# Kernel tuning notes

Measured on AMD Instinct MI355X. Metric: run time of the kernel, lower is better.

Reference implementation:

```python
import jax, jax.numpy as jnp
import numpy as np

EPS = 1e-12  # torch F.normalize eps


def _l2norm(x):
    n = jnp.sqrt(jnp.sum(x * x, axis=-1, keepdims=True))
    return x / jnp.maximum(n, EPS)


def setup_inputs() -> dict:
    key = jax.random.key(0)
    k1, k2, k3, k4 = jax.random.split(key, 4)
    Bq, Lq, Bd, Ld, H, D = 128, 32, 128, 128, 256, 128
    return {
        "query_h": jax.random.normal(k1, (Bq, Lq, H), dtype=jnp.float32),
        "doc_h": jax.random.normal(k2, (Bd, Ld, H), dtype=jnp.float32),
        "W": jax.random.normal(k3, (H, D), dtype=jnp.float32) * 0.02,
        "b": jax.random.normal(k4, (D,), dtype=jnp.float32) * 0.02,
    }


def reference(query_h, doc_h, W, b):
    # token_mapper + L2 normalize (as in embed())
    q = _l2norm(query_h @ W + b)          # [Bq, Lq, D]
    d = _l2norm(doc_h @ W + b)            # [Bd, Ld, D]
    # max_sim: cross-product bmm(doc, query^T) -> [Bq, Bd, Ld, Lq]
    scores = jnp.einsum('qsd,btd->qbts', q, d)
    # max over doc tokens (dim=1 of bmm output), sum over query tokens (dim=2)
    logits = jnp.sum(jnp.max(scores, axis=2), axis=2)  # [Bq, Bd]
    return logits
```

## Files before the change

### kernel.cpp

```cpp
#include <hip/hip_runtime.h>

typedef unsigned short u16;
typedef unsigned int u32;
typedef __attribute__((ext_vector_type(8))) short short8;
typedef __attribute__((ext_vector_type(16))) float f32x16;
typedef __attribute__((ext_vector_type(4))) float f32x4;
typedef __attribute__((ext_vector_type(4))) unsigned int u32x4;

#define H 256
#define D 128


union V16 { u32x4 u; short8 s; f32x4 f; };

static __device__ inline u32 bf16pk_rne(float a, float b) {
    u32 ua = __float_as_uint(a), ub = __float_as_uint(b);
    ua = ua + 0x7FFFu + ((ua >> 16) & 1u);
    ub = ub + 0x7FFFu + ((ub >> 16) & 1u);
    return (ua >> 16) | (ub & 0xFFFF0000u);
}

__global__ __launch_bounds__(256) void prep_w(
    const float* __restrict__ W, u16* __restrict__ whi, u16* __restrict__ wlo)
{
    const int g   = blockIdx.x * 256 + threadIdx.x;
    const int slot = g & 63;
    const int kc  = (g >> 6) & 15;
    const int nt  = g >> 10;
    const int l31 = slot >> 1;
    const int lg2 = slot & 1;
    const int k0  = kc * 16 + lg2 * 8;
    const int n   = nt * 32 + l31;

    u32 hw[4], lw[4];
    #pragma unroll
    for (int p = 0; p < 4; ++p) {
        float a = W[(size_t)(k0 + 2*p)     * D + n];
        float b = W[(size_t)(k0 + 2*p + 1) * D + n];
        u32 ua = __float_as_uint(a), ub = __float_as_uint(b);
        u32 ha = ua & 0xFFFF0000u,   hb = ub & 0xFFFF0000u;
        hw[p] = (ua >> 16) | hb;
        float la = a - __uint_as_float(ha);
        float lb = b - __uint_as_float(hb);
        u32 ra = __float_as_uint(la); ra += 0x7FFFu + ((ra >> 16) & 1u);
        u32 rb = __float_as_uint(lb); rb += 0x7FFFu + ((rb >> 16) & 1u);
        lw[p] = (ra >> 16) | (rb & 0xFFFF0000u);
    }
    u32x4 hv = {hw[0], hw[1], hw[2], hw[3]};
    u32x4 lv = {lw[0], lw[1], lw[2], lw[3]};
    *(u32x4*)&whi[(size_t)g * 8] = hv;
    *(u32x4*)&wlo[(size_t)g * 8] = lv;
}

__global__ __launch_bounds__(256) void proj_mfma(
    const float* __restrict__ Xq, const float* __restrict__ Xd,
    const float* __restrict__ bias,
    const u16* __restrict__ whi, const u16* __restrict__ wlo,
    u16* __restrict__ outq, u16* __restrict__ outd)
{
    const int tid  = threadIdx.x;
    const int wid  = tid >> 6;
    const int lane = tid & 63;
    const int l31  = lane & 31;
    const int hi   = lane >> 5;
    const int slot = l31 * 2 + hi;

    const float* X; u16* out; int trow0;
    if (blockIdx.x < 32) { X = Xq; out = outq; trow0 = blockIdx.x * 128 + wid * 32; }
    else { X = Xd; out = outd; trow0 = (blockIdx.x - 32) * 128 + wid * 32; }

    const float* xrow = X + (size_t)(trow0 + l31) * H + hi * 8;

    f32x16 acc[4];
    #pragma unroll
    for (int nt = 0; nt < 4; ++nt) acc[nt] = (f32x16){0.f};

    #pragma unroll
    for (int kc = 0; kc < 16; ++kc) {
        V16 a4, b4;
        a4.f = *(const f32x4*)(xrow + kc * 16);
        b4.f = *(const f32x4*)(xrow + kc * 16 + 4);
        float e[8];
        #pragma unroll
        for (int i = 0; i < 4; ++i) { e[i] = a4.f[i]; e[i + 4] = b4.f[i]; }

        V16 xh, xl;
        u32 xhu[4], xlu[4];
        #pragma unroll
        for (int p = 0; p < 4; ++p) {
            u32 u0 = __float_as_uint(e[2*p]), u1 = __float_as_uint(e[2*p+1]);
            u32 h0 = u0 & 0xFFFF0000u,        h1 = u1 & 0xFFFF0000u;
            xhu[p] = (u0 >> 16) | h1;
            float l0 = e[2*p]   - __uint_as_float(h0);
            float l1 = e[2*p+1] - __uint_as_float(h1);
            xlu[p] = (__float_as_uint(l0) >> 16) |
                     (__float_as_uint(l1) & 0xFFFF0000u);
        }
        xh.u = (u32x4){xhu[0], xhu[1], xhu[2], xhu[3]};
        xl.u = (u32x4){xlu[0], xlu[1], xlu[2], xlu[3]};

        #pragma unroll
        for (int nt = 0; nt < 4; ++nt) {
            V16 wh, wl;
            const size_t fo = (size_t)((nt * 16 + kc) * 64 + slot) * 8;
            wh.u = *(const u32x4*)&whi[fo];
            wl.u = *(const u32x4*)&wlo[fo];
            acc[nt] = __builtin_amdgcn_mfma_f32_32x32x16_bf16(wh.s, xh.s, acc[nt], 0, 0, 0);
            acc[nt] = __builtin_amdgcn_mfma_f32_32x32x16_bf16(wl.s, xh.s, acc[nt], 0, 0, 0);
            acc[nt] = __builtin_amdgcn_mfma_f32_32x32x16_bf16(wh.s, xl.s, acc[nt], 0, 0, 0);
        }
    }

    float ss = 0.f;
    #pragma unroll
    for (int nt = 0; nt < 4; ++nt) {
        #pragma unroll
        for (int q = 0; q < 4; ++q) {
            f32x4 b4 = *(const f32x4*)&bias[nt * 32 + q * 8 + hi * 4];
            #pragma unroll
            for (int i = 0; i < 4; ++i) {
                float v = acc[nt][q*4+i] + b4[i];
                acc[nt][q*4+i] = v;
                ss += v * v;
            }
        }
    }
    ss += __shfl_xor(ss, 32);
    const float inv = 1.0f / fmaxf(sqrtf(ss), 1e-12f);

    const size_t base = (size_t)(trow0 >> 5) * 4096;
    #pragma unroll
    for (int nt = 0; nt < 4; ++nt) {
        #pragma unroll
        for (int q = 0; q < 4; ++q) {
            float v0 = acc[nt][q*4+0] * inv, v1 = acc[nt][q*4+1] * inv;
            float v2 = acc[nt][q*4+2] * inv, v3 = acc[nt][q*4+3] * inv;
            u32 p0 = bf16pk_rne(v0, v1), p1 = bf16pk_rne(v2, v3);
            u32 r0 = __shfl_xor(p0, 32), r1 = __shfl_xor(p1, 32);
            if ((q & 1) == hi) {
                const int kc = nt * 2 + (q >> 1);
                u32x4 ck;
                if (hi == 0) ck = (u32x4){p0, p1, r0, r1};
                else         ck = (u32x4){r0, r1, p0, p1};
                *(u32x4*)&out[base + (size_t)kc * 512 + (size_t)slot * 8] = ck;
            }
        }
    }
}

__global__ __launch_bounds__(256) void maxsim_kernel(
    const u16* __restrict__ qbf, const u16* __restrict__ dbf,
    float* __restrict__ logits)
{
    __shared__ float smax[4][8][2][32];
    const int tid  = threadIdx.x;
    const int wid  = tid >> 6;
    const int lane = tid & 63;
    const int l31  = lane & 31;
    const int soff = ((lane & 31) * 2 + (lane >> 5)) * 8;

    const int qb0 = (blockIdx.x >> 4) * 2;
    const int db0 = (blockIdx.x & 15) * 8;

    short8 bq[2][8];
    #pragma unroll
    for (int qs = 0; qs < 2; ++qs) {
        const u16* qb_base = qbf + (size_t)(qb0 + qs) * 4096 + soff;
        #pragma unroll
        for (int kc = 0; kc < 8; ++kc)
            bq[qs][kc] = *(const short8*)(qb_base + kc * 512);
    }

    #pragma unroll 2
    for (int dbi = 0; dbi < 8; ++dbi) {
        const u16* dt = dbf + (size_t)((db0 + dbi) * 4 + wid) * 4096 + soff;
        short8 af[8];
        #pragma unroll
        for (int kc = 0; kc < 8; ++kc)
            af[kc] = *(const short8*)(dt + kc * 512);

        f32x16 acc0 = {0.f}, acc1 = {0.f};
        #pragma unroll
        for (int kc = 0; kc < 8; ++kc) {
            acc0 = __builtin_amdgcn_mfma_f32_32x32x16_bf16(af[kc], bq[0][kc], acc0, 0, 0, 0);
            acc1 = __builtin_amdgcn_mfma_f32_32x32x16_bf16(af[kc], bq[1][kc], acc1, 0, 0, 0);
        }

        #pragma unroll
        for (int qs = 0; qs < 2; ++qs) {
            const f32x16 a = qs ? acc1 : acc0;
            float m0 = fmaxf(a[0], a[1]),   m1 = fmaxf(a[2], a[3]);
            float m2 = fmaxf(a[4], a[5]),   m3 = fmaxf(a[6], a[7]);
            float m4 = fmaxf(a[8], a[9]),   m5 = fmaxf(a[10], a[11]);
            float m6 = fmaxf(a[12], a[13]), m7 = fmaxf(a[14], a[15]);
            float m = fmaxf(fmaxf(fmaxf(m0, m1), fmaxf(m2, m3)),
                            fmaxf(fmaxf(m4, m5), fmaxf(m6, m7)));
            m = fmaxf(m, __shfl_xor(m, 32));
            if (lane < 32) smax[wid][dbi][qs][l31] = m;
        }
    }
    __syncthreads();

    {
        const int dbi = tid >> 5;
        const int col = tid & 31;
        float v0 = fmaxf(fmaxf(smax[0][dbi][0][col], smax[1][dbi][0][col]),
                         fmaxf(smax[2][dbi][0][col], smax[3][dbi][0][col]));
        float v1 = fmaxf(fmaxf(smax[0][dbi][1][col], smax[1][dbi][1][col]),
                         fmaxf(smax[2][dbi][1][col], smax[3][dbi][1][col]));
        v0 += __shfl_xor(v0, 1);  v1 += __shfl_xor(v1, 1);
        v0 += __shfl_xor(v0, 2);  v1 += __shfl_xor(v1, 2);
        v0 += __shfl_xor(v0, 4);  v1 += __shfl_xor(v1, 4);
        v0 += __shfl_xor(v0, 8);  v1 += __shfl_xor(v1, 8);
        v0 += __shfl_xor(v0, 16); v1 += __shfl_xor(v1, 16);
        if (col == 0) {
            logits[(size_t)qb0 * 128 + db0 + dbi]       = v0;
            logits[(size_t)(qb0 + 1) * 128 + db0 + dbi] = v1;
        }
    }
}

extern "C" void kernel_launch(void* const* d_in, const int* in_sizes, int n_in,
                              void* d_out, int out_size, void* d_ws, size_t ws_size,
                              hipStream_t stream)
{
    const float* query_h = (const float*)d_in[0];
    const float* doc_h   = (const float*)d_in[1];
    const float* W       = (const float*)d_in[2];
    const float* bias    = (const float*)d_in[3];
    float* logits = (float*)d_out;

    u16* qbf = (u16*)d_ws;
    u16* dbf = qbf + (size_t)128 * 4096;
    u16* whi = dbf + (size_t)512 * 4096;
    u16* wlo = whi + (size_t)4096 * 8;

    prep_w   <<<dim3(16),   dim3(256), 0, stream>>>(W, whi, wlo);
    proj_mfma<<<dim3(160),  dim3(256), 0, stream>>>(query_h, doc_h, bias, whi, wlo, qbf, dbf);
    maxsim_kernel<<<dim3(1024), dim3(256), 0, stream>>>(qbf, dbf, logits);
}
```

Before: 105.5 us.

## Stage projection inputs through swizzled LDS and double-buffer doc fragment loads

The projection kernel now has each wavefront copy its 32 input rows into a 32 KB-per-wave shared buffer with coalesced row loads and an XOR swizzle. MFMA operands are then read from LDS instead of issuing strided per-lane global reads. The maxsim kernel is restructured to double-buffer the doc fragment registers, prefetching the next doc tile while the current one is multiplied. This trades 128 KB of LDS per block (limiting occupancy) and more registers for better global coalescing and load/compute overlap.

Measured after the change: 104.3 us. Within noise of the previous version (-1.2%).

```diff
diff --git a/kernel.cpp b/kernel.cpp
--- a/kernel.cpp
+++ b/kernel.cpp
@@ -58,6 +58,7 @@
     const u16* __restrict__ whi, const u16* __restrict__ wlo,
     u16* __restrict__ outq, u16* __restrict__ outd)
 {
+    __shared__ float xst[4][32][256];
     const int tid  = threadIdx.x;
     const int wid  = tid >> 6;
     const int lane = tid & 63;
@@ -69,20 +70,31 @@
     if (blockIdx.x < 32) { X = Xq; out = outq; trow0 = blockIdx.x * 128 + wid * 32; }
     else { X = Xd; out = outd; trow0 = (blockIdx.x - 32) * 128 + wid * 32; }
 
-    const float* xrow = X + (size_t)(trow0 + l31) * H + hi * 8;
+    {
+        float* xw = &xst[wid][0][0];
+        const float* xs0 = X + (size_t)trow0 * H;
+        #pragma unroll
+        for (int t = 0; t < 32; ++t) {
+            f32x4 v = *(const f32x4*)&xs0[(size_t)t * H + lane * 4];
+            int sl = lane ^ (t & 7);
+            *(f32x4*)&xw[t * 256 + sl * 4] = v;
+        }
+    }
 
     f32x16 acc[4];
     #pragma unroll
     for (int nt = 0; nt < 4; ++nt) acc[nt] = (f32x16){0.f};
 
+    const float* xw = &xst[wid][0][0];
     #pragma unroll
     for (int kc = 0; kc < 16; ++kc) {
-        V16 a4, b4;
-        a4.f = *(const f32x4*)(xrow + kc * 16);
-        b4.f = *(const f32x4*)(xrow + kc * 16 + 4);
+        const int g = kc * 4 + hi * 2;
+        const int sw = l31 & 7;
+        f32x4 va = *(const f32x4*)&xw[l31 * 256 + ((g ^ sw) << 2)];
+        f32x4 vb = *(const f32x4*)&xw[l31 * 256 + (((g + 1) ^ sw) << 2)];
         float e[8];
         #pragma unroll
-        for (int i = 0; i < 4; ++i) { e[i] = a4.f[i]; e[i + 4] = b4.f[i]; }
+        for (int i = 0; i < 4; ++i) { e[i] = va[i]; e[i + 4] = vb[i]; }
 
         V16 xh, xl;
         u32 xhu[4], xlu[4];
@@ -148,6 +160,39 @@
     }
 }
 
+
+#define LOAD_AF(AF, DBI)                                                       \
+    {                                                                          \
+        const u16* dt_ = dbf + (size_t)((db0 + (DBI)) * 4 + wid) * 4096 + soff;\
+        _Pragma("unroll")                                                      \
+        for (int kc = 0; kc < 8; ++kc)                                         \
+            AF[kc] = *(const short8*)(dt_ + kc * 512);                         \
+    }
+
+#define COMPUTE_AF(AF, DBI)                                                    \
+    {                                                                          \
+        f32x16 acc0 = {0.f}, acc1 = {0.f};                                     \
+        _Pragma("unroll")                                                      \
+        for (int kc = 0; kc < 8; ++kc) {                                       \
+            acc0 = __builtin_amdgcn_mfma_f32_32x32x16_bf16(AF[kc], bq[0][kc],  \
+                                                           acc0, 0, 0, 0);     \
+            acc1 = __builtin_amdgcn_mfma_f32_32x32x16_bf16(AF[kc], bq[1][kc],  \
+                                                           acc1, 0, 0, 0);     \
+        }                                                                      \
+        _Pragma("unroll")                                                      \
+        for (int qs = 0; qs < 2; ++qs) {                                       \
+            const f32x16 a = qs ? acc1 : acc0;                                 \
+            float m0 = fmaxf(a[0], a[1]),   m1 = fmaxf(a[2], a[3]);            \
+            float m2 = fmaxf(a[4], a[5]),   m3 = fmaxf(a[6], a[7]);            \
+            float m4 = fmaxf(a[8], a[9]),   m5 = fmaxf(a[10], a[11]);          \
+            float m6 = fmaxf(a[12], a[13]), m7 = fmaxf(a[14], a[15]);          \
+            float m = fmaxf(fmaxf(fmaxf(m0, m1), fmaxf(m2, m3)),               \
+                            fmaxf(fmaxf(m4, m5), fmaxf(m6, m7)));              \
+            m = fmaxf(m, __shfl_xor(m, 32));                                   \
+            if (lane < 32) smax[wid][DBI][qs][l31] = m;                        \
+        }                                                                      \
+    }
+
 __global__ __launch_bounds__(256) void maxsim_kernel(
     const u16* __restrict__ qbf, const u16* __restrict__ dbf,
     float* __restrict__ logits)
@@ -171,33 +216,14 @@
             bq[qs][kc] = *(const short8*)(qb_base + kc * 512);
     }
 
-    #pragma unroll 2
-    for (int dbi = 0; dbi < 8; ++dbi) {
-        const u16* dt = dbf + (size_t)((db0 + dbi) * 4 + wid) * 4096 + soff;
-        short8 af[8];
-        #pragma unroll
-        for (int kc = 0; kc < 8; ++kc)
-            af[kc] = *(const short8*)(dt + kc * 512);
-
-        f32x16 acc0 = {0.f}, acc1 = {0.f};
-        #pragma unroll
-        for (int kc = 0; kc < 8; ++kc) {
-            acc0 = __builtin_amdgcn_mfma_f32_32x32x16_bf16(af[kc], bq[0][kc], acc0, 0, 0, 0);
-            acc1 = __builtin_amdgcn_mfma_f32_32x32x16_bf16(af[kc], bq[1][kc], acc1, 0, 0, 0);
-        }
-
-        #pragma unroll
-        for (int qs = 0; qs < 2; ++qs) {
-            const f32x16 a = qs ? acc1 : acc0;
-            float m0 = fmaxf(a[0], a[1]),   m1 = fmaxf(a[2], a[3]);
-            float m2 = fmaxf(a[4], a[5]),   m3 = fmaxf(a[6], a[7]);
-            float m4 = fmaxf(a[8], a[9]),   m5 = fmaxf(a[10], a[11]);
-            float m6 = fmaxf(a[12], a[13]), m7 = fmaxf(a[14], a[15]);
-            float m = fmaxf(fmaxf(fmaxf(m0, m1), fmaxf(m2, m3)),
-                            fmaxf(fmaxf(m4, m5), fmaxf(m6, m7)));
-            m = fmaxf(m, __shfl_xor(m, 32));
-            if (lane < 32) smax[wid][dbi][qs][l31] = m;
-        }
+    short8 afA[8], afB[8];
+    LOAD_AF(afA, 0);
+    #pragma unroll
+    for (int dbi = 0; dbi < 8; dbi += 2) {
+        LOAD_AF(afB, dbi + 1);
+        COMPUTE_AF(afA, dbi);
+        if (dbi + 2 < 8) LOAD_AF(afA, dbi + 2);
+        COMPUTE_AF(afB, dbi + 1);
     }
     __syncthreads();
 
```

## Stage projection input through swizzled LDS and restructure maxsim per-wave doc ownership

Applied to the files above, without the earlier changes.

The projection kernel now runs one wave per block over 640 blocks. Each block first loads its 32 rows into shared memory with coalesced, XOR-swizzled stores, so the per-lane strided global reads are avoided and more blocks can be spread across CUs. The maxsim kernel now has each wave own one whole doc batch and compute it against 4 query batches held in LDS, keeping running maxima in registers. This removes the shared-memory cross-wave max reduction and the extra block-wide sync. The trade-off is repeated LDS reads of the query fragments for every tile, and 32KB of LDS per block, which may limit occupancy.

Measured after the change: 108.3 us. 1.03x slower.

```diff
diff --git a/kernel.cpp b/kernel.cpp
--- a/kernel.cpp
+++ b/kernel.cpp
@@ -52,24 +52,31 @@
     *(u32x4*)&wlo[(size_t)g * 8] = lv;
 }
 
-__global__ __launch_bounds__(256) void proj_mfma(
+__global__ __launch_bounds__(64) void proj_mfma(
     const float* __restrict__ Xq, const float* __restrict__ Xd,
     const float* __restrict__ bias,
     const u16* __restrict__ whi, const u16* __restrict__ wlo,
     u16* __restrict__ outq, u16* __restrict__ outd)
 {
-    const int tid  = threadIdx.x;
-    const int wid  = tid >> 6;
-    const int lane = tid & 63;
+    __shared__ float xst[32][256];
+    const int lane = threadIdx.x & 63;
     const int l31  = lane & 31;
     const int hi   = lane >> 5;
     const int slot = l31 * 2 + hi;
 
     const float* X; u16* out; int trow0;
-    if (blockIdx.x < 32) { X = Xq; out = outq; trow0 = blockIdx.x * 128 + wid * 32; }
-    else { X = Xd; out = outd; trow0 = (blockIdx.x - 32) * 128 + wid * 32; }
-
-    const float* xrow = X + (size_t)(trow0 + l31) * H + hi * 8;
+    if (blockIdx.x < 128) { X = Xq; out = outq; trow0 = blockIdx.x * 32; }
+    else { X = Xd; out = outd; trow0 = (blockIdx.x - 128) * 32; }
+
+    {
+        const float* xs0 = X + (size_t)trow0 * H;
+        #pragma unroll
+        for (int t = 0; t < 32; ++t) {
+            f32x4 v = *(const f32x4*)&xs0[(size_t)t * H + lane * 4];
+            int sl = lane ^ (t & 7);
+            *(f32x4*)&xst[t][sl * 4] = v;
+        }
+    }
 
     f32x16 acc[4];
     #pragma unroll
@@ -77,12 +84,13 @@
 
     #pragma unroll
     for (int kc = 0; kc < 16; ++kc) {
-        V16 a4, b4;
-        a4.f = *(const f32x4*)(xrow + kc * 16);
-        b4.f = *(const f32x4*)(xrow + kc * 16 + 4);
+        const int g = kc * 4 + hi * 2;
+        const int sw = l31 & 7;
+        f32x4 va = *(const f32x4*)&xst[l31][((g ^ sw) << 2)];
+        f32x4 vb = *(const f32x4*)&xst[l31][(((g + 1) ^ sw) << 2)];
         float e[8];
         #pragma unroll
-        for (int i = 0; i < 4; ++i) { e[i] = a4.f[i]; e[i + 4] = b4.f[i]; }
+        for (int i = 0; i < 4; ++i) { e[i] = va[i]; e[i + 4] = vb[i]; }
 
         V16 xh, xl;
         u32 xhu[4], xlu[4];
@@ -138,11 +146,11 @@
             u32 p0 = bf16pk_rne(v0, v1), p1 = bf16pk_rne(v2, v3);
             u32 r0 = __shfl_xor(p0, 32), r1 = __shfl_xor(p1, 32);
             if ((q & 1) == hi) {
-                const int kc = nt * 2 + (q >> 1);
+                const int kcs = nt * 2 + (q >> 1);
                 u32x4 ck;
                 if (hi == 0) ck = (u32x4){p0, p1, r0, r1};
                 else         ck = (u32x4){r0, r1, p0, p1};
-                *(u32x4*)&out[base + (size_t)kc * 512 + (size_t)slot * 8] = ck;
+                *(u32x4*)&out[base + (size_t)kcs * 512 + (size_t)slot * 8] = ck;
             }
         }
     }
@@ -152,71 +160,69 @@
     const u16* __restrict__ qbf, const u16* __restrict__ dbf,
     float* __restrict__ logits)
 {
-    __shared__ float smax[4][8][2][32];
+    __shared__ u16 qlds[4 * 4096];
     const int tid  = threadIdx.x;
     const int wid  = tid >> 6;
     const int lane = tid & 63;
-    const int l31  = lane & 31;
     const int soff = ((lane & 31) * 2 + (lane >> 5)) * 8;
 
-    const int qb0 = (blockIdx.x >> 4) * 2;
-    const int db0 = (blockIdx.x & 15) * 8;
-
-    short8 bq[2][8];
-    #pragma unroll
-    for (int qs = 0; qs < 2; ++qs) {
-        const u16* qb_base = qbf + (size_t)(qb0 + qs) * 4096 + soff;
+    const int qg  = blockIdx.x >> 5;
+    const int dg  = blockIdx.x & 31;
+    const int qb0 = qg * 4;
+    const int dbg = dg * 4 + wid;
+
+    {
+        const u32x4* src = (const u32x4*)(qbf + (size_t)qb0 * 4096);
+        u32x4* dst = (u32x4*)qlds;
+        #pragma unroll
+        for (int i = 0; i < 8; ++i)
+            dst[tid + i * 256] = src[tid + i * 256];
+    }
+    __syncthreads();
+
+    float rmax[4] = {-3.4e38f, -3.4e38f, -3.4e38f, -3.4e38f};
+    const u16* dbase = dbf + (size_t)dbg * 4 * 4096 + soff;
+
+    #pragma unroll
+    for (int tile = 0; tile < 4; ++tile) {
+        short8 af[8];
         #pragma unroll
         for (int kc = 0; kc < 8; ++kc)
-            bq[qs][kc] = *(const short8*)(qb_base + kc * 512);
-    }
-
-    #pragma unroll 2
-    for (int dbi = 0; dbi < 8; ++dbi) {
-        const u16* dt = dbf + (size_t)((db0 + dbi) * 4 + wid) * 4096 + soff;
-        short8 af[8];
-        #pragma unroll
-        for (int kc = 0; kc < 8; ++kc)
-            af[kc] = *(const short8*)(dt + kc * 512);
-
-        f32x16 acc0 = {0.f}, acc1 = {0.f};
-        #pragma unroll
-        for (int kc = 0; kc < 8; ++kc) {
-            acc0 = __builtin_amdgcn_mfma_f32_32x32x16_bf16(af[kc], bq[0][kc], acc0, 0, 0, 0);
-            acc1 = __builtin_amdgcn_mfma_f32_32x32x16_bf16(af[kc], bq[1][kc], acc1, 0, 0, 0);
-        }
-
-        #pragma unroll
-        for (int qs = 0; qs < 2; ++qs) {
-            const f32x16 a = qs ? acc1 : acc0;
-            float m0 = fmaxf(a[0], a[1]),   m1 = fmaxf(a[2], a[3]);
-            float m2 = fmaxf(a[4], a[5]),   m3 = fmaxf(a[6], a[7]);
-            float m4 = fmaxf(a[8], a[9]),   m5 = fmaxf(a[10], a[11]);
-            float m6 = fmaxf(a[12], a[13]), m7 = fmaxf(a[14], a[15]);
-            float m = fmaxf(fmaxf(fmaxf(m0, m1), fmaxf(m2, m3)),
-                            fmaxf(fmaxf(m4, m5), fmaxf(m6, m7)));
-            m = fmaxf(m, __shfl_xor(m, 32));
-            if (lane < 32) smax[wid][dbi][qs][l31] = m;
-        }
-    }
-    __syncthreads();
-
-    {
-        const int dbi = tid >> 5;
-        const int col = tid & 31;
-        float v0 = fmaxf(fmaxf(smax[0][dbi][0][col], smax[1][dbi][0][col]),
-                         fmaxf(smax[2][dbi][0][col], smax[3][dbi][0][col]));
-        float v1 = fmaxf(fmaxf(smax[0][dbi][1][col], smax[1][dbi][1][col]),
-                         fmaxf(smax[2][dbi][1][col], smax[3][dbi][1][col]));
-        v0 += __shfl_xor(v0, 1);  v1 += __shfl_xor(v1, 1);
-        v0 += __shfl_xor(v0, 2);  v1 += __shfl_xor(v1, 2);
-        v0 += __shfl_xor(v0, 4);  v1 += __shfl_xor(v1, 4);
-        v0 += __shfl_xor(v0, 8);  v1 += __shfl_xor(v1, 8);
-        v0 += __shfl_xor(v0, 16); v1 += __shfl_xor(v1, 16);
-        if (col == 0) {
-            logits[(size_t)qb0 * 128 + db0 + dbi]       = v0;
-            logits[(size_t)(qb0 + 1) * 128 + db0 + dbi] = v1;
-        }
+            af[kc] = *(const short8*)(dbase + (size_t)tile * 4096 + kc * 512);
+
+        #pragma unroll
+        for (int qp = 0; qp < 2; ++qp) {
+            f32x16 a0 = {0.f}, a1 = {0.f};
+            #pragma unroll
+            for (int kc = 0; kc < 8; ++kc) {
+                short8 b0 = *(const short8*)&qlds[(qp*2+0)*4096 + kc*512 + soff];
+                short8 b1 = *(const short8*)&qlds[(qp*2+1)*4096 + kc*512 + soff];
+                a0 = __builtin_amdgcn_mfma_f32_32x32x16_bf16(af[kc], b0, a0, 0, 0, 0);
+                a1 = __builtin_amdgcn_mfma_f32_32x32x16_bf16(af[kc], b1, a1, 0, 0, 0);
+            }
+            #pragma unroll
+            for (int h = 0; h < 2; ++h) {
+                const f32x16 a = h ? a1 : a0;
+                float m0 = fmaxf(a[0], a[1]),   m1 = fmaxf(a[2], a[3]);
+                float m2 = fmaxf(a[4], a[5]),   m3 = fmaxf(a[6], a[7]);
+                float m4 = fmaxf(a[8], a[9]),   m5 = fmaxf(a[10], a[11]);
+                float m6 = fmaxf(a[12], a[13]), m7 = fmaxf(a[14], a[15]);
+                float m = fmaxf(fmaxf(fmaxf(m0, m1), fmaxf(m2, m3)),
+                                fmaxf(fmaxf(m4, m5), fmaxf(m6, m7)));
+                rmax[qp*2+h] = fmaxf(rmax[qp*2+h], m);
+            }
+        }
+    }
+
+    #pragma unroll
+    for (int qs = 0; qs < 4; ++qs) {
+        float v = fmaxf(rmax[qs], __shfl_xor(rmax[qs], 32));
+        v += __shfl_xor(v, 1);
+        v += __shfl_xor(v, 2);
+        v += __shfl_xor(v, 4);
+        v += __shfl_xor(v, 8);
+        v += __shfl_xor(v, 16);
+        if (lane == 0) logits[(size_t)(qb0 + qs) * 128 + dbg] = v;
     }
 }
 
@@ -236,6 +242,6 @@
     u16* wlo = whi + (size_t)4096 * 8;
 
     prep_w   <<<dim3(16),   dim3(256), 0, stream>>>(W, whi, wlo);
-    proj_mfma<<<dim3(160),  dim3(256), 0, stream>>>(query_h, doc_h, bias, whi, wlo, qbf, dbf);
+    proj_mfma<<<dim3(640),  dim3(64),  0, stream>>>(query_h, doc_h, bias, whi, wlo, qbf, dbf);
     maxsim_kernel<<<dim3(1024), dim3(256), 0, stream>>>(qbf, dbf, logits);
 }
```
